# Kernel optimization log

Hardware: AMD Instinct MI355X
Metric: run time of the kernel (lower is better)

## Reference

```python
import jax, jax.numpy as jnp
import numpy as np

B, S, ENC, DEC, ATT = 32, 2048, 1024, 1024, 1024


def setup_inputs() -> dict:
    key = jax.random.key(0)
    k1, k2, k3, k4, k5, k6 = jax.random.split(key, 6)
    sc = lambda fan_in: 1.0 / np.sqrt(fan_in)
    return {
        "encoder_hidden_states": jax.random.normal(k1, (B, S, ENC), dtype=jnp.float32),
        "decoder_hidden_state": jax.random.normal(k2, (B, 1, DEC), dtype=jnp.float32),
        # nn.Linear stores weight as [out, in]; we keep [in, out] for x @ W
        "U_a": jax.random.uniform(k3, (ENC, ATT), jnp.float32, -sc(ENC), sc(ENC)),
        "W_a": jax.random.uniform(k4, (DEC, ATT), jnp.float32, -sc(DEC), sc(DEC)),
        "v_t": jax.random.uniform(k5, (ATT, 1), jnp.float32, -sc(ATT), sc(ATT)),
        "ffn": jax.random.uniform(k6, (ENC + DEC, DEC), jnp.float32, -sc(ENC + DEC), sc(ENC + DEC)),
    }


def reference(encoder_hidden_states, decoder_hidden_state, U_a, W_a, v_t, ffn):
    # additive (Bahdanau) attention
    u = jnp.einsum('bse,ea->bsa', encoder_hidden_states, U_a)      # [B,S,A]
    w = jnp.einsum('bqd,da->bqa', decoder_hidden_state, W_a)       # [B,1,A]
    e = jnp.tanh(w + u) @ v_t                                      # [B,S,1]
    align = jax.nn.softmax(e, axis=1)                              # softmax over seq
    # context = alignment^T @ encoder_states  -> [B,1,E]
    context = jnp.einsum('bsq,bse->bqe', align, encoder_hidden_states)
    cat = jnp.concatenate([decoder_hidden_state, context], axis=-1)  # [B,1,D+E]
    output = jnp.tanh(cat @ ffn)                                     # [B,1,D]
    return (output, context)
```

## Files before the change

kernel.cpp:

```cpp
#include <hip/hip_runtime.h>
#include <hip/hip_bf16.h>
#include <cstdint>
#include <cstddef>

#define B_  32
#define S_  2048
#define E_  1024
#define A_  1024
#define D_  1024
#define M_TOT (B_ * S_)

typedef __attribute__((ext_vector_type(8))) __bf16 bf16x8;
typedef __attribute__((ext_vector_type(4))) float  f32x4;

__device__ __forceinline__ float fast_tanh(float x) {
    float cx = fminf(fmaxf(x, -15.f), 15.f);
    float e2 = __expf(2.f * cx);
    return 1.f - 2.f / (e2 + 1.f);
}

__device__ __forceinline__ bf16x8 cvt8(const float* __restrict__ p) {
    float4 f0 = *(const float4*)p;
    float4 f1 = *(const float4*)(p + 4);
    bf16x8 r;
    r[0] = (__bf16)f0.x; r[1] = (__bf16)f0.y; r[2] = (__bf16)f0.z; r[3] = (__bf16)f0.w;
    r[4] = (__bf16)f1.x; r[5] = (__bf16)f1.y; r[6] = (__bf16)f1.z; r[7] = (__bf16)f1.w;
    return r;
}

typedef __attribute__((address_space(3))) uint32_t lds_u32_t;
typedef __attribute__((address_space(1))) const uint32_t gbl_u32_t;
__device__ __forceinline__ void async_ld16(const void* g, void* l) {
    __builtin_amdgcn_global_load_lds((gbl_u32_t*)g,
                                     (lds_u32_t*)(uint32_t)(uintptr_t)l,
                                     16, 0, 0);
}

__global__ __launch_bounds__(256) void k_convert_enc(const float* __restrict__ enc,
                                                     __bf16* __restrict__ xb) {
    size_t idx = ((size_t)blockIdx.x * 256 + threadIdx.x) * 8;
    *(bf16x8*)(xb + idx) = cvt8(enc + idx);
}

__global__ __launch_bounds__(256) void k_prep(const float* __restrict__ Ua,
                                              __bf16* __restrict__ Ut,
                                              const float* __restrict__ ffn,
                                              float* __restrict__ ffnT) {
    int bid = blockIdx.x;
    if (bid < 4096) {
        int idx = bid * 256 + threadIdx.x;
        int k = idx >> 10, n = idx & 1023;
        Ut[n * 1024 + k] = (__bf16)Ua[idx];
    } else {
        int idx = (bid - 4096) * 256 + threadIdx.x;
        int i = idx >> 10, d = idx & 1023;
        ffnT[(size_t)d * 2048 + i] = ffn[idx];
    }
}

__global__ __launch_bounds__(256) void k_w_part(const float* __restrict__ dec,
                                                const float* __restrict__ Wa,
                                                float* __restrict__ w_part) {
    int bid = blockIdx.x;
    int ac = bid & 3, b = (bid >> 2) & 31, kc = bid >> 7;
    int a = ac * 256 + threadIdx.x;
    int k0 = kc * 128;
    float acc = 0.f;
    #pragma unroll 8
    for (int k = 0; k < 128; ++k)
        acc += dec[b * 1024 + k0 + k] * Wa[(size_t)(k0 + k) * 1024 + a];
    w_part[kc * 32768 + b * 1024 + a] = acc;
}

template <bool USE_XB>
__global__ __launch_bounds__(256) void k_gemm_e(
        const float* __restrict__ enc, const __bf16* __restrict__ Xb,
        const __bf16* __restrict__ Ut, const float* __restrict__ w_part,
        const float* __restrict__ v, float* __restrict__ e_part) {
    __shared__ __bf16 lX[128 * 32];
    __shared__ __bf16 lU[128 * 32];
    __shared__ float  e_lds[2][128];

    const int t = threadIdx.x;
    const int bid = blockIdx.x;
    const int xcd = bid & 7;
    const int j_  = bid >> 3;
    const int m_tile = xcd * 64 + (j_ >> 3);
    const int n_tile = j_ & 7;
    const int m0 = m_tile * 128;
    const int n0 = n_tile * 128;
    const int wave = t >> 6;
    const int lane = t & 63;
    const int q = lane >> 4;
    const int c = lane & 15;
    const int wm = (wave >> 1) * 64;
    const int wn = (wave & 1) * 64;

    f32x4 acc[4][4];
    #pragma unroll
    for (int i = 0; i < 4; ++i)
        #pragma unroll
        for (int j = 0; j < 4; ++j)
            #pragma unroll
            for (int r = 0; r < 4; ++r) acc[i][j][r] = 0.f;

    const int lrow = lane >> 2;
    const int lcol = (lane & 3) * 8;
    const int xrow = wave * 32;
    const int srow = t >> 2;
    const int scol = (t & 3) * 8;

    for (int kk = 0; kk < 1024; kk += 32) {
        __syncthreads();
        if (USE_XB) {
            const __bf16* gx = Xb + (size_t)(m0 + xrow + lrow) * 1024 + kk + lcol;
            async_ld16(gx,              &lX[(xrow     ) * 32]);
            async_ld16(gx + 16 * 1024,  &lX[(xrow + 16) * 32]);
            const __bf16* gu = Ut + (size_t)(n0 + xrow + lrow) * 1024 + kk + lcol;
            async_ld16(gu,              &lU[(xrow     ) * 32]);
            async_ld16(gu + 16 * 1024,  &lU[(xrow + 16) * 32]);
        } else {
            const float* s0 = enc + (size_t)(m0 + srow) * 1024 + kk + scol;
            *(bf16x8*)(&lX[srow * 32])        = cvt8(s0);
            *(bf16x8*)(&lX[(srow + 64) * 32]) = cvt8(s0 + (size_t)64 * 1024);
            const __bf16* u0 = Ut + (size_t)(n0 + srow) * 1024 + kk + scol;
            *(int4*)(&lU[srow * 32])        = *(const int4*)u0;
            *(int4*)(&lU[(srow + 64) * 32]) = *(const int4*)(u0 + 64 * 1024);
        }
        __syncthreads();

        bf16x8 af[4], bfr[4];
        #pragma unroll
        for (int i = 0; i < 4; ++i)
            af[i] = *(const bf16x8*)(&lX[(wm + i * 16 + c) * 32 + q * 8]);
        #pragma unroll
        for (int j = 0; j < 4; ++j)
            bfr[j] = *(const bf16x8*)(&lU[(wn + j * 16 + c) * 32 + q * 8]);
        #pragma unroll
        for (int i = 0; i < 4; ++i)
            #pragma unroll
            for (int j = 0; j < 4; ++j)
                acc[i][j] = __builtin_amdgcn_mfma_f32_16x16x32_bf16(af[i], bfr[j], acc[i][j], 0, 0, 0);
    }

    const int b_idx = m0 >> 11;
    float wv[4], vv[4];
    #pragma unroll
    for (int j = 0; j < 4; ++j) {
        int col = n0 + wn + j * 16 + c;
        float s = 0.f;
        #pragma unroll
        for (int p = 0; p < 8; ++p) s += w_part[p * 32768 + b_idx * 1024 + col];
        wv[j] = s;
        vv[j] = v[col];
    }
    #pragma unroll
    for (int i = 0; i < 4; ++i) {
        float s0 = 0.f, s1 = 0.f, s2 = 0.f, s3 = 0.f;
        #pragma unroll
        for (int j = 0; j < 4; ++j) {
            s0 += fast_tanh(wv[j] + acc[i][j][0]) * vv[j];
            s1 += fast_tanh(wv[j] + acc[i][j][1]) * vv[j];
            s2 += fast_tanh(wv[j] + acc[i][j][2]) * vv[j];
            s3 += fast_tanh(wv[j] + acc[i][j][3]) * vv[j];
        }
        #pragma unroll
        for (int off = 1; off < 16; off <<= 1) {
            s0 += __shfl_xor(s0, off, 16);
            s1 += __shfl_xor(s1, off, 16);
            s2 += __shfl_xor(s2, off, 16);
            s3 += __shfl_xor(s3, off, 16);
        }
        if (c == 0) {
            int row = wm + i * 16 + q * 4;
            e_lds[wave & 1][row + 0] = s0;
            e_lds[wave & 1][row + 1] = s1;
            e_lds[wave & 1][row + 2] = s2;
            e_lds[wave & 1][row + 3] = s3;
        }
    }
    __syncthreads();
    if (t < 128)
        e_part[(size_t)n_tile * M_TOT + m0 + t] = e_lds[0][t] + e_lds[1][t];
}

__global__ __launch_bounds__(256) void k_softmax(const float* __restrict__ ep,
                                                 float* __restrict__ al) {
    int b = blockIdx.x, t = threadIdx.x;
    float ev[8];
    #pragma unroll
    for (int i = 0; i < 8; ++i) {
        int s = i * 256 + t;
        float x = 0.f;
        #pragma unroll
        for (int p = 0; p < 8; ++p) x += ep[p * M_TOT + b * 2048 + s];
        ev[i] = x;
    }
    float mx = ev[0];
    #pragma unroll
    for (int i = 1; i < 8; ++i) mx = fmaxf(mx, ev[i]);
    #pragma unroll
    for (int off = 1; off < 64; off <<= 1) mx = fmaxf(mx, __shfl_xor(mx, off, 64));
    __shared__ float redm[4];
    if ((t & 63) == 0) redm[t >> 6] = mx;
    __syncthreads();
    mx = fmaxf(fmaxf(redm[0], redm[1]), fmaxf(redm[2], redm[3]));

    float ex[8], sm = 0.f;
    #pragma unroll
    for (int i = 0; i < 8; ++i) { ex[i] = __expf(ev[i] - mx); sm += ex[i]; }
    #pragma unroll
    for (int off = 1; off < 64; off <<= 1) sm += __shfl_xor(sm, off, 64);
    __shared__ float reds[4];
    if ((t & 63) == 0) reds[t >> 6] = sm;
    __syncthreads();
    sm = reds[0] + reds[1] + reds[2] + reds[3];
    float inv = 1.f / sm;
    #pragma unroll
    for (int i = 0; i < 8; ++i) al[b * 2048 + i * 256 + t] = ex[i] * inv;
}

template <bool USE_XB>
__global__ __launch_bounds__(256) void k_ctx(const float* __restrict__ enc,
                                             const __bf16* __restrict__ Xb,
                                             const float* __restrict__ al,
                                             float* __restrict__ ctx_part) {
    int b  = blockIdx.x >> 5;
    int sc = blockIdx.x & 31;
    int t  = threadIdx.x;
    int sh = t >> 7;
    int e8 = (t & 127) * 8;
    float acc[8];
    #pragma unroll
    for (int r = 0; r < 8; ++r) acc[r] = 0.f;
    int rbase = sc * 64 + sh * 32;
    for (int i = 0; i < 32; i += 4) {
        #pragma unroll
        for (int u = 0; u < 4; ++u) {
            int s = rbase + i + u;
            float a = al[b * 2048 + s];
            if (USE_XB) {
                bf16x8 x = *(const bf16x8*)(Xb + (size_t)(b * 2048 + s) * 1024 + e8);
                #pragma unroll
                for (int r = 0; r < 8; ++r) acc[r] += a * (float)x[r];
            } else {
                const float* xp = enc + (size_t)(b * 2048 + s) * 1024 + e8;
                float4 x0 = *(const float4*)xp;
                float4 x1 = *(const float4*)(xp + 4);
                acc[0] += a * x0.x; acc[1] += a * x0.y; acc[2] += a * x0.z; acc[3] += a * x0.w;
                acc[4] += a * x1.x; acc[5] += a * x1.y; acc[6] += a * x1.z; acc[7] += a * x1.w;
            }
        }
    }
    float* o = ctx_part + ((size_t)(sc * 2 + sh) * 32 + b) * 1024 + e8;
    float4 r0; r0.x = acc[0]; r0.y = acc[1]; r0.z = acc[2]; r0.w = acc[3];
    float4 r1; r1.x = acc[4]; r1.y = acc[5]; r1.z = acc[6]; r1.w = acc[7];
    *(float4*)o = r0;
    *(float4*)(o + 4) = r1;
}

__global__ __launch_bounds__(256) void k_ctx_sum(const float* __restrict__ ctx_part,
                                                 float* __restrict__ ctx,
                                                 float* __restrict__ out) {
    int idx = blockIdx.x * 256 + threadIdx.x;
    float s = 0.f;
    #pragma unroll
    for (int p = 0; p < 64; ++p) s += ctx_part[(size_t)p * 32768 + idx];
    ctx[idx] = s;
    out[32768 + idx] = s;
}

__global__ __launch_bounds__(256) void k_out(const float* __restrict__ dec,
                                             const float* __restrict__ ctx,
                                             const float* __restrict__ ffnT,
                                             float* __restrict__ out) {
    int b  = blockIdx.x >> 8;
    int dg = blockIdx.x & 255;
    __shared__ float cat[2048];
    int t = threadIdx.x;
    #pragma unroll
    for (int r = 0; r < 4; ++r) {
        cat[r * 256 + t]        = dec[b * 1024 + r * 256 + t];
        cat[1024 + r * 256 + t] = ctx[b * 1024 + r * 256 + t];
    }
    __syncthreads();
    int wave = t >> 6, lane = t & 63;
    int d = dg * 4 + wave;
    float acc = 0.f;
    #pragma unroll
    for (int r = 0; r < 8; ++r) {
        int idx = r * 256 + lane * 4;
        float4 c4 = *(const float4*)(cat + idx);
        float4 f4 = *(const float4*)(ffnT + (size_t)d * 2048 + idx);
        acc += c4.x * f4.x + c4.y * f4.y + c4.z * f4.z + c4.w * f4.w;
    }
    #pragma unroll
    for (int off = 1; off < 64; off <<= 1) acc += __shfl_xor(acc, off, 64);
    if (lane == 0) out[b * 1024 + d] = fast_tanh(acc);
}

extern "C" void kernel_launch(void* const* d_in, const int* in_sizes, int n_in,
                              void* d_out, int out_size, void* d_ws, size_t ws_size,
                              hipStream_t stream) {
    const float* enc = (const float*)d_in[0];
    const float* dec = (const float*)d_in[1];
    const float* Ua  = (const float*)d_in[2];
    const float* Wa  = (const float*)d_in[3];
    const float* vt  = (const float*)d_in[4];
    const float* ffn = (const float*)d_in[5];
    float* out = (float*)d_out;

    char* ws = (char*)d_ws;
    size_t off = 0;
    __bf16* Ut       = (__bf16*)(ws + off); off += (size_t)A_ * E_ * 2;
    float*  ffnT     = (float*)(ws + off);  off += (size_t)2048 * 1024 * 4;
    float*  e_part   = (float*)(ws + off);  off += (size_t)8 * M_TOT * 4;
    float*  al       = (float*)(ws + off);  off += (size_t)M_TOT * 4;
    float*  w_part   = (float*)(ws + off);  off += (size_t)8 * B_ * 1024 * 4;
    float*  ctx_part = (float*)(ws + off);  off += (size_t)64 * B_ * 1024 * 4;
    float*  ctx      = (float*)(ws + off);  off += (size_t)B_ * 1024 * 4;
    off = (off + 255) & ~(size_t)255;
    __bf16* Xb       = (__bf16*)(ws + off);
    bool use_xb = (ws_size >= off + (size_t)M_TOT * E_ * 2);

    if (use_xb)
        k_convert_enc<<<(M_TOT * E_) / (256 * 8), 256, 0, stream>>>(enc, Xb);
    k_prep<<<4096 + 8192, 256, 0, stream>>>(Ua, Ut, ffn, ffnT);
    k_w_part<<<1024, 256, 0, stream>>>(dec, Wa, w_part);
    if (use_xb)
        k_gemm_e<true><<<4096, 256, 0, stream>>>(enc, Xb, Ut, w_part, vt, e_part);
    else
        k_gemm_e<false><<<4096, 256, 0, stream>>>(enc, Xb, Ut, w_part, vt, e_part);
    k_softmax<<<B_, 256, 0, stream>>>(e_part, al);
    if (use_xb)
        k_ctx<true><<<B_ * 32, 256, 0, stream>>>(enc, Xb, al, ctx_part);
    else
        k_ctx<false><<<B_ * 32, 256, 0, stream>>>(enc, Xb, al, ctx_part);
    k_ctx_sum<<<(B_ * 1024) / 256, 256, 0, stream>>>(ctx_part, ctx, out);
    k_out<<<B_ * 256, 256, 0, stream>>>(dec, ctx, ffnT, out);
}
```

Measured before the change: 713.0 us.

## Double-buffer GEMM LDS loads, tile U transpose, and drop ffn transpose

The score GEMM's async global-to-LDS path now double-buffers its X and U tiles, so the next K-slice loads while MFMAs run on the current one. U_a is transposed through a padded LDS tile instead of a scattered strided write. The full fp32 ffn transpose is gone: the output projection reads ffn rows directly in a split-K kernel and a small reduce kernel applies tanh. This removes about 16MB of transpose traffic and reduces GEMM load stalls, at the cost of double the GEMM LDS footprint and one extra launch.

```diff
diff --git a/kernel.cpp b/kernel.cpp
--- a/kernel.cpp
+++ b/kernel.cpp
@@ -42,20 +42,20 @@
     *(bf16x8*)(xb + idx) = cvt8(enc + idx);
 }
 
-__global__ __launch_bounds__(256) void k_prep(const float* __restrict__ Ua,
-                                              __bf16* __restrict__ Ut,
-                                              const float* __restrict__ ffn,
-                                              float* __restrict__ ffnT) {
+__global__ __launch_bounds__(256) void k_trans_U(const float* __restrict__ Ua,
+                                                 __bf16* __restrict__ Ut) {
+    __shared__ float tile[64][65];
     int bid = blockIdx.x;
-    if (bid < 4096) {
-        int idx = bid * 256 + threadIdx.x;
-        int k = idx >> 10, n = idx & 1023;
-        Ut[n * 1024 + k] = (__bf16)Ua[idx];
-    } else {
-        int idx = (bid - 4096) * 256 + threadIdx.x;
-        int i = idx >> 10, d = idx & 1023;
-        ffnT[(size_t)d * 2048 + i] = ffn[idx];
-    }
+    int k0 = (bid >> 4) * 64, n0 = (bid & 15) * 64;
+    int t = threadIdx.x;
+    int r = t >> 6, c = t & 63;
+    #pragma unroll
+    for (int i = 0; i < 16; ++i)
+        tile[i * 4 + r][c] = Ua[(size_t)(k0 + i * 4 + r) * 1024 + n0 + c];
+    __syncthreads();
+    #pragma unroll
+    for (int i = 0; i < 16; ++i)
+        Ut[(size_t)(n0 + i * 4 + r) * 1024 + k0 + c] = (__bf16)tile[c][i * 4 + r];
 }
 
 __global__ __launch_bounds__(256) void k_w_part(const float* __restrict__ dec,
@@ -77,8 +77,8 @@
         const float* __restrict__ enc, const __bf16* __restrict__ Xb,
         const __bf16* __restrict__ Ut, const float* __restrict__ w_part,
         const float* __restrict__ v, float* __restrict__ e_part) {
-    __shared__ __bf16 lX[128 * 32];
-    __shared__ __bf16 lU[128 * 32];
+    __shared__ __bf16 lX[2][128 * 32];
+    __shared__ __bf16 lU[2][128 * 32];
     __shared__ float  e_lds[2][128];
 
     const int t = threadIdx.x;
@@ -107,40 +107,67 @@
     const int lrow = lane >> 2;
     const int lcol = (lane & 3) * 8;
     const int xrow = wave * 32;
-    const int srow = t >> 2;
-    const int scol = (t & 3) * 8;
-
-    for (int kk = 0; kk < 1024; kk += 32) {
+
+    if (USE_XB) {
+        const __bf16* gxb = Xb + (size_t)(m0 + xrow + lrow) * 1024 + lcol;
+        const __bf16* gub = Ut + (size_t)(n0 + xrow + lrow) * 1024 + lcol;
+
+        auto stage = [&](int kk, int bsel) {
+            async_ld16(gxb + kk,             &lX[bsel][xrow * 32]);
+            async_ld16(gxb + kk + 16 * 1024, &lX[bsel][(xrow + 16) * 32]);
+            async_ld16(gub + kk,             &lU[bsel][xrow * 32]);
+            async_ld16(gub + kk + 16 * 1024, &lU[bsel][(xrow + 16) * 32]);
+        };
+        auto compute = [&](int bsel) {
+            bf16x8 af[4], bfr[4];
+            #pragma unroll
+            for (int i = 0; i < 4; ++i)
+                af[i] = *(const bf16x8*)(&lX[bsel][(wm + i * 16 + c) * 32 + q * 8]);
+            #pragma unroll
+            for (int j = 0; j < 4; ++j)
+                bfr[j] = *(const bf16x8*)(&lU[bsel][(wn + j * 16 + c) * 32 + q * 8]);
+            #pragma unroll
+            for (int i = 0; i < 4; ++i)
+                #pragma unroll
+                for (int j = 0; j < 4; ++j)
+                    acc[i][j] = __builtin_amdgcn_mfma_f32_16x16x32_bf16(af[i], bfr[j], acc[i][j], 0, 0, 0);
+        };
+
+        stage(0, 0);
         __syncthreads();
-        if (USE_XB) {
-            const __bf16* gx = Xb + (size_t)(m0 + xrow + lrow) * 1024 + kk + lcol;
-            async_ld16(gx,              &lX[(xrow     ) * 32]);
-            async_ld16(gx + 16 * 1024,  &lX[(xrow + 16) * 32]);
-            const __bf16* gu = Ut + (size_t)(n0 + xrow + lrow) * 1024 + kk + lcol;
-            async_ld16(gu,              &lU[(xrow     ) * 32]);
-            async_ld16(gu + 16 * 1024,  &lU[(xrow + 16) * 32]);
-        } else {
+        for (int kk = 0; kk < 1024; kk += 64) {
+            if (kk + 32 < 1024) stage(kk + 32, 1);
+            compute(0);
+            __syncthreads();
+            if (kk + 64 < 1024) stage(kk + 64, 0);
+            compute(1);
+            __syncthreads();
+        }
+    } else {
+        const int srow = t >> 2;
+        const int scol = (t & 3) * 8;
+        for (int kk = 0; kk < 1024; kk += 32) {
+            __syncthreads();
             const float* s0 = enc + (size_t)(m0 + srow) * 1024 + kk + scol;
-            *(bf16x8*)(&lX[srow * 32])        = cvt8(s0);
-            *(bf16x8*)(&lX[(srow + 64) * 32]) = cvt8(s0 + (size_t)64 * 1024);
+            *(bf16x8*)(&lX[0][srow * 32])        = cvt8(s0);
+            *(bf16x8*)(&lX[0][(srow + 64) * 32]) = cvt8(s0 + (size_t)64 * 1024);
             const __bf16* u0 = Ut + (size_t)(n0 + srow) * 1024 + kk + scol;
-            *(int4*)(&lU[srow * 32])        = *(const int4*)u0;
-            *(int4*)(&lU[(srow + 64) * 32]) = *(const int4*)(u0 + 64 * 1024);
-        }
-        __syncthreads();
-
-        bf16x8 af[4], bfr[4];
-        #pragma unroll
-        for (int i = 0; i < 4; ++i)
-            af[i] = *(const bf16x8*)(&lX[(wm + i * 16 + c) * 32 + q * 8]);
-        #pragma unroll
-        for (int j = 0; j < 4; ++j)
-            bfr[j] = *(const bf16x8*)(&lU[(wn + j * 16 + c) * 32 + q * 8]);
-        #pragma unroll
-        for (int i = 0; i < 4; ++i)
+            *(int4*)(&lU[0][srow * 32])        = *(const int4*)u0;
+            *(int4*)(&lU[0][(srow + 64) * 32]) = *(const int4*)(u0 + 64 * 1024);
+            __syncthreads();
+            bf16x8 af[4], bfr[4];
+            #pragma unroll
+            for (int i = 0; i < 4; ++i)
+                af[i] = *(const bf16x8*)(&lX[0][(wm + i * 16 + c) * 32 + q * 8]);
             #pragma unroll
             for (int j = 0; j < 4; ++j)
-                acc[i][j] = __builtin_amdgcn_mfma_f32_16x16x32_bf16(af[i], bfr[j], acc[i][j], 0, 0, 0);
+                bfr[j] = *(const bf16x8*)(&lU[0][(wn + j * 16 + c) * 32 + q * 8]);
+            #pragma unroll
+            for (int i = 0; i < 4; ++i)
+                #pragma unroll
+                for (int j = 0; j < 4; ++j)
+                    acc[i][j] = __builtin_amdgcn_mfma_f32_16x16x32_bf16(af[i], bfr[j], acc[i][j], 0, 0, 0);
+        }
     }
 
     const int b_idx = m0 >> 11;
@@ -270,33 +297,38 @@
     out[32768 + idx] = s;
 }
 
-__global__ __launch_bounds__(256) void k_out(const float* __restrict__ dec,
-                                             const float* __restrict__ ctx,
-                                             const float* __restrict__ ffnT,
-                                             float* __restrict__ out) {
-    int b  = blockIdx.x >> 8;
-    int dg = blockIdx.x & 255;
-    __shared__ float cat[2048];
+__global__ __launch_bounds__(256) void k_out_part(const float* __restrict__ dec,
+                                                  const float* __restrict__ ctx,
+                                                  const float* __restrict__ ffn,
+                                                  float* __restrict__ out_part) {
+    int bid = blockIdx.x;
+    int b = bid & 31, kc = bid >> 5;
     int t = threadIdx.x;
-    #pragma unroll
-    for (int r = 0; r < 4; ++r) {
-        cat[r * 256 + t]        = dec[b * 1024 + r * 256 + t];
-        cat[1024 + r * 256 + t] = ctx[b * 1024 + r * 256 + t];
-    }
-    __syncthreads();
-    int wave = t >> 6, lane = t & 63;
-    int d = dg * 4 + wave;
-    float acc = 0.f;
-    #pragma unroll
-    for (int r = 0; r < 8; ++r) {
-        int idx = r * 256 + lane * 4;
-        float4 c4 = *(const float4*)(cat + idx);
-        float4 f4 = *(const float4*)(ffnT + (size_t)d * 2048 + idx);
-        acc += c4.x * f4.x + c4.y * f4.y + c4.z * f4.z + c4.w * f4.w;
-    }
-    #pragma unroll
-    for (int off = 1; off < 64; off <<= 1) acc += __shfl_xor(acc, off, 64);
-    if (lane == 0) out[b * 1024 + d] = fast_tanh(acc);
+    __shared__ float catl[256];
+    int i0 = kc * 256;
+    catl[t] = (i0 < 1024) ? dec[b * 1024 + i0 + t] : ctx[b * 1024 + i0 - 1024 + t];
+    __syncthreads();
+    float a0 = 0.f, a1 = 0.f, a2 = 0.f, a3 = 0.f;
+    #pragma unroll 4
+    for (int i = 0; i < 256; ++i) {
+        float cv = catl[i];
+        const float* fr = ffn + (size_t)(i0 + i) * 1024;
+        a0 += cv * fr[t];
+        a1 += cv * fr[t + 256];
+        a2 += cv * fr[t + 512];
+        a3 += cv * fr[t + 768];
+    }
+    float* o = out_part + ((size_t)kc * 32 + b) * 1024;
+    o[t] = a0; o[t + 256] = a1; o[t + 512] = a2; o[t + 768] = a3;
+}
+
+__global__ __launch_bounds__(256) void k_out_final(const float* __restrict__ out_part,
+                                                   float* __restrict__ out) {
+    int idx = blockIdx.x * 256 + threadIdx.x;
+    float s = 0.f;
+    #pragma unroll
+    for (int p = 0; p < 8; ++p) s += out_part[(size_t)p * 32768 + idx];
+    out[idx] = fast_tanh(s);
 }
 
 extern "C" void kernel_launch(void* const* d_in, const int* in_sizes, int n_in,
@@ -313,19 +345,19 @@
     char* ws = (char*)d_ws;
     size_t off = 0;
     __bf16* Ut       = (__bf16*)(ws + off); off += (size_t)A_ * E_ * 2;
-    float*  ffnT     = (float*)(ws + off);  off += (size_t)2048 * 1024 * 4;
     float*  e_part   = (float*)(ws + off);  off += (size_t)8 * M_TOT * 4;
     float*  al       = (float*)(ws + off);  off += (size_t)M_TOT * 4;
     float*  w_part   = (float*)(ws + off);  off += (size_t)8 * B_ * 1024 * 4;
     float*  ctx_part = (float*)(ws + off);  off += (size_t)64 * B_ * 1024 * 4;
     float*  ctx      = (float*)(ws + off);  off += (size_t)B_ * 1024 * 4;
+    float*  out_part = (float*)(ws + off);  off += (size_t)8 * B_ * 1024 * 4;
     off = (off + 255) & ~(size_t)255;
     __bf16* Xb       = (__bf16*)(ws + off);
     bool use_xb = (ws_size >= off + (size_t)M_TOT * E_ * 2);
 
     if (use_xb)
         k_convert_enc<<<(M_TOT * E_) / (256 * 8), 256, 0, stream>>>(enc, Xb);
-    k_prep<<<4096 + 8192, 256, 0, stream>>>(Ua, Ut, ffn, ffnT);
+    k_trans_U<<<256, 256, 0, stream>>>(Ua, Ut);
     k_w_part<<<1024, 256, 0, stream>>>(dec, Wa, w_part);
     if (use_xb)
         k_gemm_e<true><<<4096, 256, 0, stream>>>(enc, Xb, Ut, w_part, vt, e_part);
@@ -337,5 +369,6 @@
     else
         k_ctx<false><<<B_ * 32, 256, 0, stream>>>(enc, Xb, al, ctx_part);
     k_ctx_sum<<<(B_ * 1024) / 256, 256, 0, stream>>>(ctx_part, ctx, out);
-    k_out<<<B_ * 256, 256, 0, stream>>>(dec, ctx, ffnT, out);
-}
+    k_out_part<<<256, 256, 0, stream>>>(dec, ctx, ffn, out_part);
+    k_out_final<<<(B_ * 1024) / 256, 256, 0, stream>>>(out_part, out);
+}
```

Result: no change. 701.4 us (-1.6%).
